# Kernel optimization log

Hardware: AMD Instinct MI355X
Metric: run time of the kernel (lower is better)

Reference implementation:

```python
import jax, jax.numpy as jnp
import numpy as np

B, H, C, PX, PY = 2, 16, 4, 16, 16
EXTRA = 64
HD = 64
N = C * PX * PY + EXTRA


def setup_inputs() -> dict:
    key = jax.random.key(0)
    ks = jax.random.split(key, 8)
    q = jax.random.normal(ks[0], (B, H, N, HD), jnp.float32)
    k = jax.random.normal(ks[1], (B, H, N, HD), jnp.float32)
    v = jax.random.normal(ks[2], (B, H, N, HD), jnp.float32)
    # valid SE(3) world-to-camera matrices: rotation via QR (det fixed to +1)
    A = jax.random.normal(ks[3], (B, C, 3, 3), jnp.float32)
    Q, _ = jnp.linalg.qr(A)
    det = jnp.linalg.det(Q)
    Q = Q * det[..., None, None]
    t = 0.5 * jax.random.normal(ks[4], (B, C, 3), jnp.float32)
    top = jnp.concatenate([Q, t[..., None]], -1)
    bot = jnp.broadcast_to(jnp.array([0.0, 0.0, 0.0, 1.0], jnp.float32), (B, C, 1, 4))
    viewmats = jnp.concatenate([top, bot], -2)
    # pinhole intrinsics (no skew)
    fx = 300.0 + 10.0 * jax.random.uniform(ks[5], (B, C))
    fy = 300.0 + 10.0 * jax.random.uniform(ks[6], (B, C))
    z = jnp.zeros((B, C)); o = jnp.ones((B, C))
    cx = 128.0 * o; cy = 128.0 * o
    Ks = jnp.stack([jnp.stack([fx, z, cx], -1), jnp.stack([z, fy, cy], -1), jnp.stack([z, z, o], -1)], -2)
    spatial_mask = jnp.arange(N) >= EXTRA  # first EXTRA tokens are non-spatial
    return {"q": q, "k": k, "v": v, "viewmats": viewmats, "Ks": Ks,
            "spatial_mask": spatial_mask, "patches_x": PX, "patches_y": PY,
            "image_width": 256, "image_height": 256}


def _invert_SE3(T):
    R = T[..., :3, :3]; t = T[..., :3, 3]
    Rinv = jnp.swapaxes(R, -1, -2)
    tinv = -jnp.einsum('...ij,...j->...i', Rinv, t)
    top = jnp.concatenate([Rinv, tinv[..., None]], -1)
    bot = jnp.broadcast_to(jnp.array([0.0, 0.0, 0.0, 1.0], T.dtype), T.shape[:-2] + (1, 4))
    return jnp.concatenate([top, bot], -2)


def _lift(K3):
    out = jnp.zeros(K3.shape[:-2] + (4, 4), K3.dtype)
    return out.at[..., :3, :3].set(K3).at[..., 3, 3].set(1.0)


def _invert_K(K):
    fx = K[..., 0, 0]; fy = K[..., 1, 1]; cx = K[..., 0, 2]; cy = K[..., 1, 2]
    z = jnp.zeros_like(fx); o = jnp.ones_like(fx)
    return jnp.stack([jnp.stack([1.0 / fx, z, -cx / fx], -1),
                      jnp.stack([z, 1.0 / fy, -cy / fy], -1),
                      jnp.stack([z, z, o], -1)], -2)


def _transform(feats, M, cosx, sinx, cosy, siny, inverse):
    # Block-diagonal: [tiled 4x4 projmat on D/2 | RoPE-x on D/4 | RoPE-y on D/4]
    Bq, Hq, Nq, D = feats.shape
    h2 = D // 2; h4 = D // 4
    p = feats[..., :h2].reshape(Bq, Hq, Nq, h2 // 4, 4)
    p = jnp.einsum('bnij,bhnkj->bhnki', M, p).reshape(Bq, Hq, Nq, h2)

    def rope(x, c, s):
        c = c[None, None]; s = s[None, None]  # [1,1,N,nf]
        xa, xb = x[..., : x.shape[-1] // 2], x[..., x.shape[-1] // 2:]
        if inverse:
            return jnp.concatenate([c * xa - s * xb, s * xa + c * xb], -1)
        return jnp.concatenate([c * xa + s * xb, -s * xa + c * xb], -1)

    rx = rope(feats[..., h2:h2 + h4], cosx, sinx)
    ry = rope(feats[..., h2 + h4:], cosy, siny)
    return jnp.concatenate([p, rx, ry], -1)


def reference(q, k, v, viewmats, Ks, spatial_mask, patches_x, patches_y, image_width, image_height):
    D = q.shape[-1]
    Bq, Cq = viewmats.shape[:2]
    # normalized intrinsics
    fx = Ks[..., 0, 0] / image_width; fy = Ks[..., 1, 1] / image_height
    cx = Ks[..., 0, 2] / image_width - 0.5; cy = Ks[..., 1, 2] / image_height - 0.5
    z = jnp.zeros_like(fx); o = jnp.ones_like(fx)
    Kn = jnp.stack([jnp.stack([fx, z, cx], -1), jnp.stack([z, fy, cy], -1), jnp.stack([z, z, o], -1)], -2)
    P = jnp.einsum('...ij,...jk->...ik', _lift(Kn), viewmats)          # [B,C,4,4]
    P_T = jnp.swapaxes(P, -1, -2)
    P_inv = jnp.einsum('...ij,...jk->...ik', _invert_SE3(viewmats), _lift(_invert_K(Kn)))
    # RoPE tables over spatial tokens (split convention, base=100, scale=1)
    nf = D // 8
    freqs = 100.0 ** (-jnp.arange(nf, dtype=jnp.float32) / nf)
    pos_x = jnp.tile(jnp.arange(patches_x, dtype=jnp.float32), patches_y * Cq)
    pos_y = jnp.tile(jnp.repeat(jnp.arange(patches_y, dtype=jnp.float32), patches_x), Cq)
    ang_x = pos_x[:, None] * freqs; ang_y = pos_y[:, None] * freqs  # [S,nf]
    mask = spatial_mask
    S = pos_x.shape[0]
    # index of each token within the spatial-token ordering (masked scatter, vectorized)
    sidx = jnp.clip(jnp.cumsum(mask.astype(jnp.int32)) - 1, 0, S - 1)
    m = mask[:, None]
    cosx = jnp.where(m, jnp.cos(ang_x)[sidx], 1.0); sinx = jnp.where(m, jnp.sin(ang_x)[sidx], 0.0)
    cosy = jnp.where(m, jnp.cos(ang_y)[sidx], 1.0); siny = jnp.where(m, jnp.sin(ang_y)[sidx], 0.0)
    cam = sidx // (patches_x * patches_y)  # camera id per token
    I4 = jnp.eye(4, dtype=q.dtype)
    mm = mask[None, :, None, None]
    Mq = jnp.where(mm, P_T[:, cam], I4)    # [B,N,4,4]
    Mkv = jnp.where(mm, P_inv[:, cam], I4)
    Mo = jnp.where(mm, P[:, cam], I4)
    qt = _transform(q, Mq, cosx, sinx, cosy, siny, False)
    kt = _transform(k, Mkv, cosx, sinx, cosy, siny, False)
    vt = _transform(v, Mkv, cosx, sinx, cosy, siny, False)
    logits = jnp.einsum('bhqd,bhkd->bhqk', qt, kt) / jnp.sqrt(jnp.float32(D))
    attn = jax.nn.softmax(logits, axis=-1)
    out = jnp.einsum('bhqk,bhkd->bhqd', attn, vt)
    return _transform(out, Mo, cosx, sinx, cosy, siny, True)
```

## Files before the change

kernel.cpp:

```cpp
#include <hip/hip_runtime.h>
#include <math.h>

typedef _Float16 f16;
typedef _Float16 f16x8 __attribute__((ext_vector_type(8)));
typedef __fp16 h16x2 __attribute__((ext_vector_type(2)));
typedef float f32x16 __attribute__((ext_vector_type(16)));
typedef unsigned int u32;
typedef u32 u32x4 __attribute__((ext_vector_type(4)));

constexpr int Bc = 2, Hc = 16, Cc = 4, PXc = 16, PYc = 16, EXTRAc = 64, HDc = 64;
constexpr int Nc = Cc * PXc * PYc + EXTRAc;
constexpr int BH = Bc * Hc;
constexpr int KT = 64;
constexpr int NKT = Nc / KT;
constexpr int KS = 4;
constexpr int NQT = Nc / 32;
constexpr int NBLK = NQT * BH * KS;

constexpr size_t TENS_SZ  = (size_t)BH * Nc * HDc * 2;
constexpr size_t PBH      = (size_t)Nc * 128;
constexpr size_t QF_OFF   = 0;
constexpr size_t KF_OFF   = QF_OFF + TENS_SZ;
constexpr size_t VT_OFF   = KF_OFF + TENS_SZ;
constexpr size_t PART_OFF = VT_OFF + TENS_SZ;
constexpr size_t ML_OFF   = PART_OFF + (size_t)KS * TENS_SZ;

__device__ const float FREQS[8] = {1.0f, 0.5623413252f, 0.31622776601f, 0.17782794100f,
                                   0.1f, 0.05623413252f, 0.031622776602f, 0.017782794100f};
constexpr float QSCALE = 0.125f * 1.4426950408889634f;

__device__ __forceinline__ void compute_M(float* M, const float* __restrict__ vm,
                                          const float* __restrict__ Ks3, int b, int cam, int which) {
    const float* V  = vm + (b * Cc + cam) * 16;
    const float* K3 = Ks3 + (b * Cc + cam) * 9;
    float fx = K3[0] * (1.0f / 256.0f);
    float fy = K3[4] * (1.0f / 256.0f);
    float cx = K3[2] * (1.0f / 256.0f) - 0.5f;
    float cy = K3[5] * (1.0f / 256.0f) - 0.5f;
    if (which == 2) {
        float IV[16];
        IV[0] = V[0]; IV[1] = V[4]; IV[2] = V[8];
        IV[4] = V[1]; IV[5] = V[5]; IV[6] = V[9];
        IV[8] = V[2]; IV[9] = V[6]; IV[10] = V[10];
        float tx = V[3], ty = V[7], tz = V[11];
        IV[3]  = -(IV[0] * tx + IV[1] * ty + IV[2] * tz);
        IV[7]  = -(IV[4] * tx + IV[5] * ty + IV[6] * tz);
        IV[11] = -(IV[8] * tx + IV[9] * ty + IV[10] * tz);
        IV[12] = 0.f; IV[13] = 0.f; IV[14] = 0.f; IV[15] = 1.f;
        float ifx = 1.f / fx, ify = 1.f / fy;
        float ncx = -cx * ifx, ncy = -cy * ify;
        #pragma unroll
        for (int i = 0; i < 4; ++i) {
            M[i * 4 + 0] = IV[i * 4 + 0] * ifx;
            M[i * 4 + 1] = IV[i * 4 + 1] * ify;
            M[i * 4 + 2] = IV[i * 4 + 0] * ncx + IV[i * 4 + 1] * ncy + IV[i * 4 + 2];
            M[i * 4 + 3] = IV[i * 4 + 3];
        }
    } else {
        float P[16];
        #pragma unroll
        for (int j = 0; j < 4; ++j) {
            P[0 * 4 + j] = fx * V[0 * 4 + j] + cx * V[2 * 4 + j];
            P[1 * 4 + j] = fy * V[1 * 4 + j] + cy * V[2 * 4 + j];
            P[2 * 4 + j] = V[2 * 4 + j];
            P[3 * 4 + j] = V[3 * 4 + j];
        }
        if (which == 0) {
            #pragma unroll
            for (int i = 0; i < 16; ++i) M[i] = P[i];
        } else {
            #pragma unroll
            for (int i = 0; i < 4; ++i)
                #pragma unroll
                for (int j = 0; j < 4; ++j) M[i * 4 + j] = P[j * 4 + i];
        }
    }
}

template <bool INV>
__device__ __forceinline__ void xf_seg(float* v16, int seg, int n, int b, int which,
                                       const float* __restrict__ vm, const float* __restrict__ Ks3) {
    if (n < EXTRAc) return;
    int sidx = n - EXTRAc;
    int cam = sidx >> 8;
    if (seg < 2) {
        float M[16];
        compute_M(M, vm, Ks3, b, cam, which);
        #pragma unroll
        for (int g = 0; g < 4; ++g) {
            float a0 = v16[4 * g], a1 = v16[4 * g + 1], a2 = v16[4 * g + 2], a3 = v16[4 * g + 3];
            v16[4 * g + 0] = M[0]  * a0 + M[1]  * a1 + M[2]  * a2 + M[3]  * a3;
            v16[4 * g + 1] = M[4]  * a0 + M[5]  * a1 + M[6]  * a2 + M[7]  * a3;
            v16[4 * g + 2] = M[8]  * a0 + M[9]  * a1 + M[10] * a2 + M[11] * a3;
            v16[4 * g + 3] = M[12] * a0 + M[13] * a1 + M[14] * a2 + M[15] * a3;
        }
    } else {
        float pos = (seg == 2) ? (float)(sidx & (PXc - 1)) : (float)((sidx >> 4) & (PYc - 1));
        #pragma unroll
        for (int f = 0; f < 8; ++f) {
            float s, c;
            __sincosf(pos * FREQS[f], &s, &c);
            float xa = v16[f], xb = v16[8 + f];
            if (INV) {
                v16[f]     = c * xa - s * xb;
                v16[8 + f] = s * xa + c * xb;
            } else {
                v16[f]     = c * xa + s * xb;
                v16[8 + f] = -s * xa + c * xb;
            }
        }
    }
}

__device__ __forceinline__ u32 pkh(float a, float b) {
    h16x2 r = __builtin_amdgcn_cvt_pkrtz(a, b);
    return __builtin_bit_cast(u32, r);
}

__device__ __forceinline__ f32x16 zero16() {
    f32x16 z = {0.f,0.f,0.f,0.f,0.f,0.f,0.f,0.f,0.f,0.f,0.f,0.f,0.f,0.f,0.f,0.f};
    return z;
}

__global__ void prope_xform_kernel(const float* __restrict__ q, const float* __restrict__ k,
                                   const float* __restrict__ v,
                                   const float* __restrict__ viewmats, const float* __restrict__ Ks,
                                   char* __restrict__ wsb) {
    __shared__ f16 tile[64][72];
    if (blockIdx.x < 1088) {
        int id = blockIdx.x * 256 + threadIdx.x;
        int seg = id & 3;
        int rid = id >> 2;
        int tensor = rid / (BH * Nc);
        int row = rid - tensor * (BH * Nc);
        int n = row % Nc;
        int bhq = row / Nc;
        int b = bhq >> 4;
        const float* src = (tensor ? k : q) + (size_t)row * 64 + seg * 16;
        float vals[16];
        #pragma unroll
        for (int i = 0; i < 4; ++i) ((float4*)vals)[i] = ((const float4*)src)[i];
        xf_seg<false>(vals, seg, n, b, tensor ? 2 : 1, viewmats, Ks);
        float scale = tensor ? 1.0f : QSCALE;
        f16 o[16];
        #pragma unroll
        for (int i = 0; i < 16; ++i) o[i] = (f16)(vals[i] * scale);
        if (tensor == 0) {
            char* base = wsb + QF_OFF + (size_t)bhq * PBH + (size_t)(n >> 5) * 4096;
            int qq = n & 31;
            *(float4*)(base + (seg * 2 + 0) * 512 + qq * 16) = ((float4*)o)[0];
            *(float4*)(base + (seg * 2 + 1) * 512 + qq * 16) = ((float4*)o)[1];
        } else {
            char* base = wsb + KF_OFF + (size_t)bhq * PBH + (size_t)(n >> 6) * 8192;
            int kk = n & 63, rh = kk >> 5, qq = kk & 31;
            *(float4*)(base + (((seg * 2 + rh) * 2 + 0) * 32 + qq) * 16) = ((float4*)o)[0];
            *(float4*)(base + (((seg * 2 + rh) * 2 + 1) * 32 + qq) * 16) = ((float4*)o)[1];
        }
    } else {
        int vb = blockIdx.x - 1088;
        int kt = vb >> 5, bh = vb & 31;
        int b = bh >> 4;
        int t = threadIdx.x;
        {
            int r = t >> 2, seg = t & 3;
            int n = kt * 64 + r;
            const float* src = v + ((size_t)bh * Nc + n) * 64 + seg * 16;
            float vals[16];
            #pragma unroll
            for (int i = 0; i < 4; ++i) ((float4*)vals)[i] = ((const float4*)src)[i];
            xf_seg<false>(vals, seg, n, b, 2, viewmats, Ks);
            #pragma unroll
            for (int i = 0; i < 16; ++i) tile[r][seg * 16 + i] = (f16)vals[i];
        }
        __syncthreads();
        {
            int d = t >> 2, ks = t & 3;
            f16 o[16];
            #pragma unroll
            for (int j = 0; j < 16; ++j) o[j] = tile[ks * 16 + j][d];
            int dh = d >> 5, dq = d & 31;
            char* base = wsb + VT_OFF + (size_t)bh * PBH + (size_t)kt * 8192;
            *(float4*)(base + (((ks * 2 + dh) * 2 + 0) * 32 + dq) * 16) = ((float4*)o)[0];
            *(float4*)(base + (((ks * 2 + dh) * 2 + 1) * 32 + dq) * 16) = ((float4*)o)[1];
        }
    }
}

struct KF { f16x8 a0[4]; f16x8 a1[4]; };

__device__ __forceinline__ void load_kf(KF& kf, const char* kb, int lane) {
    #pragma unroll
    for (int c = 0; c < 4; ++c) {
        kf.a0[c] = *(const f16x8*)(kb + (c * 2 + 0) * 1024 + lane * 16);
        kf.a1[c] = *(const f16x8*)(kb + (c * 2 + 1) * 1024 + lane * 16);
    }
}

__device__ __forceinline__ void tile_step(
    const KF& kc, KF& kn, bool pre, const char* vb, const char* kbn,
    const f16x8 (&qb)[4], int lane, int h,
    f32x16& o0, f32x16& o1, float& mrun, float& lrun)
{
    f32x16 s0 = zero16(), s1 = zero16();
    __builtin_amdgcn_s_setprio(1);
    #pragma unroll
    for (int c = 0; c < 4; ++c) {
        s0 = __builtin_amdgcn_mfma_f32_32x32x16_f16(kc.a0[c], qb[c], s0, 0, 0, 0);
        s1 = __builtin_amdgcn_mfma_f32_32x32x16_f16(kc.a1[c], qb[c], s1, 0, 0, 0);
    }
    __builtin_amdgcn_s_setprio(0);
    if (pre) load_kf(kn, kbn, lane);
    f16x8 va0[4], va1[4];
    #pragma unroll
    for (int c = 0; c < 4; ++c) {
        va0[c] = *(const f16x8*)(vb + (c * 2 + 0) * 1024 + lane * 16);
        va1[c] = *(const f16x8*)(vb + (c * 2 + 1) * 1024 + lane * 16);
    }

    float q8[8];
    #pragma unroll
    for (int i = 0; i < 4; ++i) {
        q8[i]     = fmaxf(fmaxf(s0[4*i], s0[4*i+1]), fmaxf(s0[4*i+2], s0[4*i+3]));
        q8[4 + i] = fmaxf(fmaxf(s1[4*i], s1[4*i+1]), fmaxf(s1[4*i+2], s1[4*i+3]));
    }
    float tm = fmaxf(fmaxf(fmaxf(q8[0], q8[1]), fmaxf(q8[2], q8[3])),
                     fmaxf(fmaxf(q8[4], q8[5]), fmaxf(q8[6], q8[7])));
    tm = fmaxf(tm, __shfl_xor(tm, 32, 64));
    if (!__all(tm <= mrun + 8.0f)) {
        float nm = fmaxf(mrun, tm);
        float corr = exp2f(mrun - nm);
        mrun = nm;
        lrun *= corr;
        #pragma unroll
        for (int i = 0; i < 16; ++i) { o0[i] *= corr; o1[i] *= corr; }
    }
    #pragma unroll
    for (int i = 0; i < 16; ++i) s0[i] = exp2f(s0[i] - mrun);
    #pragma unroll
    for (int i = 0; i < 16; ++i) s1[i] = exp2f(s1[i] - mrun);
    float a8[8];
    #pragma unroll
    for (int i = 0; i < 4; ++i) {
        a8[i]     = (s0[4*i] + s0[4*i+1]) + (s0[4*i+2] + s0[4*i+3]);
        a8[4 + i] = (s1[4*i] + s1[4*i+1]) + (s1[4*i+2] + s1[4*i+3]);
    }
    float ps = ((a8[0] + a8[1]) + (a8[2] + a8[3])) + ((a8[4] + a8[5]) + (a8[6] + a8[7]));
    ps += __shfl_xor(ps, 32, 64);
    lrun += ps;

    u32 U0[8], U1[8];
    #pragma unroll
    for (int g = 0; g < 4; ++g) {
        U0[g * 2 + 0] = pkh(s0[4 * g + 0], s0[4 * g + 1]);
        U0[g * 2 + 1] = pkh(s0[4 * g + 2], s0[4 * g + 3]);
        U1[g * 2 + 0] = pkh(s1[4 * g + 0], s1[4 * g + 1]);
        U1[g * 2 + 1] = pkh(s1[4 * g + 2], s1[4 * g + 3]);
    }

    #pragma unroll
    for (int c = 0; c < 4; ++c) {
        const u32* Us = (c < 2) ? U0 : U1;
        int gl = 2 * (c & 1);
        u32 x0 = Us[(gl + 1) * 2 + 0], x1 = Us[(gl + 1) * 2 + 1];
        u32 y0 = Us[gl * 2 + 0],       y1 = Us[gl * 2 + 1];
        u32 s0w = h ? y0 : x0;
        u32 s1w = h ? y1 : x1;
        u32 r0 = (u32)__shfl_xor((int)s0w, 32, 64);
        u32 r1 = (u32)__shfl_xor((int)s1w, 32, 64);
        u32 own0 = h ? x0 : y0, own1 = h ? x1 : y1;
        u32 w0 = h ? r0 : own0;
        u32 w1 = h ? r1 : own1;
        u32 w2 = h ? own0 : r0;
        u32 w3 = h ? own1 : r1;
        u32x4 fw = {w0, w1, w2, w3};
        f16x8 pb = __builtin_bit_cast(f16x8, fw);
        __builtin_amdgcn_s_setprio(1);
        o0 = __builtin_amdgcn_mfma_f32_32x32x16_f16(va0[c], pb, o0, 0, 0, 0);
        o1 = __builtin_amdgcn_mfma_f32_32x32x16_f16(va1[c], pb, o1, 0, 0, 0);
        __builtin_amdgcn_s_setprio(0);
    }
}

__global__ __launch_bounds__(64, 2) void prope_attn_mfma_kernel(
    const char* __restrict__ wsb, char* __restrict__ partO, float* __restrict__ partML) {
    __shared__ char ob[4096];

    const int lane = threadIdx.x;
    const int q = lane & 31, h = lane >> 5;
    const int bid = blockIdx.x;
    const int l = (bid & 7) * (NBLK / 8) + (bid >> 3);
    const int qt = l % NQT;
    const int r  = l / NQT;
    const int bh = r & 31, z = r >> 5;
    const int ts = (NKT * z) / KS, te = (NKT * (z + 1)) / KS;

    const char* kfb = wsb + KF_OFF + (size_t)bh * PBH;
    const char* vfb = wsb + VT_OFF + (size_t)bh * PBH;
    const char* qfb = wsb + QF_OFF + (size_t)bh * PBH + (size_t)qt * 4096;

    f16x8 qb[4];
    #pragma unroll
    for (int c = 0; c < 4; ++c) qb[c] = *(const f16x8*)(qfb + c * 1024 + lane * 16);

    f32x16 o0 = zero16(), o1 = zero16();
    float mrun = -1e30f, lrun = 0.f;

    KF kA, kB;
    load_kf(kA, kfb + (size_t)ts * 8192, lane);
    int it = ts;
    for (;;) {
        tile_step(kA, kB, it + 1 < te, vfb + (size_t)it * 8192,
                  kfb + (size_t)(it + 1) * 8192, qb, lane, h, o0, o1, mrun, lrun);
        if (++it >= te) break;
        tile_step(kB, kA, it + 1 < te, vfb + (size_t)it * 8192,
                  kfb + (size_t)(it + 1) * 8192, qb, lane, h, o0, o1, mrun, lrun);
        if (++it >= te) break;
    }

    float invl = 1.f / lrun;
    #pragma unroll
    for (int g = 0; g < 4; ++g) {
        #pragma unroll
        for (int w = 0; w < 2; ++w) {
            u32 u0 = pkh(o0[4 * g + 2 * w] * invl, o0[4 * g + 2 * w + 1] * invl);
            u32 u1 = pkh(o1[4 * g + 2 * w] * invl, o1[4 * g + 2 * w + 1] * invl);
            int col0 = 16 * g + 8 * h + 4 * w;
            *(u32*)(ob + ((q * 128 + col0) ^ ((q & 7) << 4))) = u0;
            *(u32*)(ob + ((q * 128 + col0 + 64) ^ ((q & 7) << 4))) = u1;
        }
    }
    if (h == 0) {
        float2 mlv = {mrun, lrun};
        ((float2*)partML)[((size_t)z * BH + bh) * Nc + qt * 32 + q] = mlv;
    }
    __syncthreads();
    {
        int rr = lane >> 1, half = lane & 1;
        char* dst = partO + (((size_t)z * BH + bh) * Nc + qt * 32 + rr) * 128 + half * 64;
        #pragma unroll
        for (int j = 0; j < 4; ++j) {
            float4 val = *(float4*)(ob + ((rr * 128 + half * 64 + j * 16) ^ ((rr & 7) << 4)));
            ((float4*)dst)[j] = val;
        }
    }
}

__global__ void prope_combine_kernel(const char* __restrict__ wsb,
                                     const float* __restrict__ viewmats, const float* __restrict__ Ks,
                                     float* __restrict__ out) {
    int id = blockIdx.x * 256 + threadIdx.x;
    int seg = id & 3, rid = id >> 2;
    int n = rid % Nc, bh = rid / Nc, b = bh >> 4;
    const float2* ml = (const float2*)(wsb + ML_OFF);
    float m[KS], l[KS];
    float mstar = -1e30f;
    #pragma unroll
    for (int s = 0; s < KS; ++s) {
        float2 v = ml[((size_t)s * BH + bh) * Nc + n];
        m[s] = v.x; l[s] = v.y;
        mstar = fmaxf(mstar, m[s]);
    }
    float wsum = 0.f, wgt[KS];
    #pragma unroll
    for (int s = 0; s < KS; ++s) { wgt[s] = exp2f(m[s] - mstar) * l[s]; wsum += wgt[s]; }
    float inv = 1.f / wsum;
    float acc[16];
    #pragma unroll
    for (int i = 0; i < 16; ++i) acc[i] = 0.f;
    #pragma unroll
    for (int s = 0; s < KS; ++s) {
        const char* op = wsb + PART_OFF + (((size_t)s * BH + bh) * Nc + n) * 128 + seg * 32;
        f16x8 a0 = *(const f16x8*)op;
        f16x8 a1 = *(const f16x8*)(op + 16);
        #pragma unroll
        for (int i = 0; i < 8; ++i) acc[i] += wgt[s] * (float)a0[i];
        #pragma unroll
        for (int i = 0; i < 8; ++i) acc[8 + i] += wgt[s] * (float)a1[i];
    }
    #pragma unroll
    for (int i = 0; i < 16; ++i) acc[i] *= inv;
    xf_seg<true>(acc, seg, n, b, 0, viewmats, Ks);
    float* go = out + ((size_t)bh * Nc + n) * 64 + seg * 16;
    #pragma unroll
    for (int i = 0; i < 4; ++i) ((float4*)go)[i] = ((const float4*)acc)[i];
}

extern "C" void kernel_launch(void* const* d_in, const int* in_sizes, int n_in,
                              void* d_out, int out_size, void* d_ws, size_t ws_size,
                              hipStream_t stream) {
    const float* q        = (const float*)d_in[0];
    const float* k        = (const float*)d_in[1];
    const float* v        = (const float*)d_in[2];
    const float* viewmats = (const float*)d_in[3];
    const float* Ks       = (const float*)d_in[4];
    char* wsb  = (char*)d_ws;
    float* out = (float*)d_out;

    prope_xform_kernel<<<1088 + 544, 256, 0, stream>>>(q, k, v, viewmats, Ks, wsb);
    prope_attn_mfma_kernel<<<NBLK, 64, 0, stream>>>(wsb, wsb + PART_OFF,
                                                    (float*)(wsb + ML_OFF));
    prope_combine_kernel<<<(BH * Nc * 4) / 256, 256, 0, stream>>>(wsb, viewmats, Ks, out);
}
```

Measured before the change: 50.64 us.

## Split each block's KV range across four waves with in-block LDS merge

Each attention block now runs four waves instead of one. Each wave processes about one quarter of the block's KV tiles (16 splits in total), and the partial outputs are merged through shared memory with a log-sum-exp rescale before the normalized partial is written out. The explicit K-tile double-buffer prefetch is dropped, and the K and V loads are issued together at the start of each tile step. The intent is to hide memory latency through more concurrent waves rather than software pipelining, at the cost of extra LDS traffic, a block-wide barrier, and a serial merge done by wave 0.

```diff
diff --git a/kernel.cpp b/kernel.cpp
--- a/kernel.cpp
+++ b/kernel.cpp
@@ -14,6 +14,7 @@
 constexpr int KT = 64;
 constexpr int NKT = Nc / KT;
 constexpr int KS = 4;
+constexpr int NSPLIT = 16;
 constexpr int NQT = Nc / 32;
 constexpr int NBLK = NQT * BH * KS;
 
@@ -186,36 +187,27 @@
     }
 }
 
-struct KF { f16x8 a0[4]; f16x8 a1[4]; };
-
-__device__ __forceinline__ void load_kf(KF& kf, const char* kb, int lane) {
-    #pragma unroll
-    for (int c = 0; c < 4; ++c) {
-        kf.a0[c] = *(const f16x8*)(kb + (c * 2 + 0) * 1024 + lane * 16);
-        kf.a1[c] = *(const f16x8*)(kb + (c * 2 + 1) * 1024 + lane * 16);
-    }
-}
-
 __device__ __forceinline__ void tile_step(
-    const KF& kc, KF& kn, bool pre, const char* vb, const char* kbn,
-    const f16x8 (&qb)[4], int lane, int h,
+    const char* kb, const char* vb, const f16x8 (&qb)[4], int lane, int h,
     f32x16& o0, f32x16& o1, float& mrun, float& lrun)
 {
+    f16x8 ka0[4], ka1[4], va0[4], va1[4];
+    #pragma unroll
+    for (int c = 0; c < 4; ++c) {
+        ka0[c] = *(const f16x8*)(kb + (c * 2 + 0) * 1024 + lane * 16);
+        ka1[c] = *(const f16x8*)(kb + (c * 2 + 1) * 1024 + lane * 16);
+        va0[c] = *(const f16x8*)(vb + (c * 2 + 0) * 1024 + lane * 16);
+        va1[c] = *(const f16x8*)(vb + (c * 2 + 1) * 1024 + lane * 16);
+    }
+
     f32x16 s0 = zero16(), s1 = zero16();
     __builtin_amdgcn_s_setprio(1);
     #pragma unroll
     for (int c = 0; c < 4; ++c) {
-        s0 = __builtin_amdgcn_mfma_f32_32x32x16_f16(kc.a0[c], qb[c], s0, 0, 0, 0);
-        s1 = __builtin_amdgcn_mfma_f32_32x32x16_f16(kc.a1[c], qb[c], s1, 0, 0, 0);
+        s0 = __builtin_amdgcn_mfma_f32_32x32x16_f16(ka0[c], qb[c], s0, 0, 0, 0);
+        s1 = __builtin_amdgcn_mfma_f32_32x32x16_f16(ka1[c], qb[c], s1, 0, 0, 0);
     }
     __builtin_amdgcn_s_setprio(0);
-    if (pre) load_kf(kn, kbn, lane);
-    f16x8 va0[4], va1[4];
-    #pragma unroll
-    for (int c = 0; c < 4; ++c) {
-        va0[c] = *(const f16x8*)(vb + (c * 2 + 0) * 1024 + lane * 16);
-        va1[c] = *(const f16x8*)(vb + (c * 2 + 1) * 1024 + lane * 16);
-    }
 
     float q8[8];
     #pragma unroll
@@ -257,6 +249,7 @@
         U1[g * 2 + 1] = pkh(s1[4 * g + 2], s1[4 * g + 3]);
     }
 
+    u32 pw[4][4];
     #pragma unroll
     for (int c = 0; c < 4; ++c) {
         const u32* Us = (c < 2) ? U0 : U1;
@@ -268,31 +261,38 @@
         u32 r0 = (u32)__shfl_xor((int)s0w, 32, 64);
         u32 r1 = (u32)__shfl_xor((int)s1w, 32, 64);
         u32 own0 = h ? x0 : y0, own1 = h ? x1 : y1;
-        u32 w0 = h ? r0 : own0;
-        u32 w1 = h ? r1 : own1;
-        u32 w2 = h ? own0 : r0;
-        u32 w3 = h ? own1 : r1;
-        u32x4 fw = {w0, w1, w2, w3};
+        pw[c][0] = h ? r0 : own0;
+        pw[c][1] = h ? r1 : own1;
+        pw[c][2] = h ? own0 : r0;
+        pw[c][3] = h ? own1 : r1;
+    }
+
+    __builtin_amdgcn_s_setprio(1);
+    #pragma unroll
+    for (int c = 0; c < 4; ++c) {
+        u32x4 fw = {pw[c][0], pw[c][1], pw[c][2], pw[c][3]};
         f16x8 pb = __builtin_bit_cast(f16x8, fw);
-        __builtin_amdgcn_s_setprio(1);
         o0 = __builtin_amdgcn_mfma_f32_32x32x16_f16(va0[c], pb, o0, 0, 0, 0);
         o1 = __builtin_amdgcn_mfma_f32_32x32x16_f16(va1[c], pb, o1, 0, 0, 0);
-        __builtin_amdgcn_s_setprio(0);
-    }
-}
-
-__global__ __launch_bounds__(64, 2) void prope_attn_mfma_kernel(
+    }
+    __builtin_amdgcn_s_setprio(0);
+}
+
+__global__ __launch_bounds__(256, 2) void prope_attn_mfma_kernel(
     const char* __restrict__ wsb, char* __restrict__ partO, float* __restrict__ partML) {
-    __shared__ char ob[4096];
-
-    const int lane = threadIdx.x;
+    __shared__ float os[4][32][64];
+    __shared__ float mls[4][2][32];
+
+    const int tid = threadIdx.x;
+    const int wv = tid >> 6, lane = tid & 63;
     const int q = lane & 31, h = lane >> 5;
     const int bid = blockIdx.x;
-    const int l = (bid & 7) * (NBLK / 8) + (bid >> 3);
-    const int qt = l % NQT;
-    const int r  = l / NQT;
-    const int bh = r & 31, z = r >> 5;
-    const int ts = (NKT * z) / KS, te = (NKT * (z + 1)) / KS;
+    const int ll = (bid & 7) * (NBLK / 8) + (bid >> 3);
+    const int qt = ll % NQT;
+    const int rest = ll / NQT;
+    const int bh = rest & 31, z = rest >> 5;
+    const int g = z * 4 + wv;
+    const int ts = (NKT * g) / NSPLIT, te = (NKT * (g + 1)) / NSPLIT;
 
     const char* kfb = wsb + KF_OFF + (size_t)bh * PBH;
     const char* vfb = wsb + VT_OFF + (size_t)bh * PBH;
@@ -305,42 +305,60 @@
     f32x16 o0 = zero16(), o1 = zero16();
     float mrun = -1e30f, lrun = 0.f;
 
-    KF kA, kB;
-    load_kf(kA, kfb + (size_t)ts * 8192, lane);
-    int it = ts;
-    for (;;) {
-        tile_step(kA, kB, it + 1 < te, vfb + (size_t)it * 8192,
-                  kfb + (size_t)(it + 1) * 8192, qb, lane, h, o0, o1, mrun, lrun);
-        if (++it >= te) break;
-        tile_step(kB, kA, it + 1 < te, vfb + (size_t)it * 8192,
-                  kfb + (size_t)(it + 1) * 8192, qb, lane, h, o0, o1, mrun, lrun);
-        if (++it >= te) break;
-    }
-
-    float invl = 1.f / lrun;
-    #pragma unroll
-    for (int g = 0; g < 4; ++g) {
-        #pragma unroll
-        for (int w = 0; w < 2; ++w) {
-            u32 u0 = pkh(o0[4 * g + 2 * w] * invl, o0[4 * g + 2 * w + 1] * invl);
-            u32 u1 = pkh(o1[4 * g + 2 * w] * invl, o1[4 * g + 2 * w + 1] * invl);
-            int col0 = 16 * g + 8 * h + 4 * w;
-            *(u32*)(ob + ((q * 128 + col0) ^ ((q & 7) << 4))) = u0;
-            *(u32*)(ob + ((q * 128 + col0 + 64) ^ ((q & 7) << 4))) = u1;
-        }
-    }
-    if (h == 0) {
-        float2 mlv = {mrun, lrun};
-        ((float2*)partML)[((size_t)z * BH + bh) * Nc + qt * 32 + q] = mlv;
-    }
+    for (int it = ts; it < te; ++it)
+        tile_step(kfb + (size_t)it * 8192, vfb + (size_t)it * 8192,
+                  qb, lane, h, o0, o1, mrun, lrun);
+
+    #pragma unroll
+    for (int i = 0; i < 16; ++i) {
+        os[wv][i][lane]      = o0[i];
+        os[wv][16 + i][lane] = o1[i];
+    }
+    if (h == 0) { mls[wv][0][q] = mrun; mls[wv][1][q] = lrun; }
     __syncthreads();
-    {
-        int rr = lane >> 1, half = lane & 1;
-        char* dst = partO + (((size_t)z * BH + bh) * Nc + qt * 32 + rr) * 128 + half * 64;
-        #pragma unroll
-        for (int j = 0; j < 4; ++j) {
-            float4 val = *(float4*)(ob + ((rr * 128 + half * 64 + j * 16) ^ ((rr & 7) << 4)));
-            ((float4*)dst)[j] = val;
+
+    if (wv == 0) {
+        float m4[4], l4[4];
+        #pragma unroll
+        for (int w = 0; w < 4; ++w) { m4[w] = mls[w][0][q]; l4[w] = mls[w][1][q]; }
+        float mB = fmaxf(fmaxf(m4[0], m4[1]), fmaxf(m4[2], m4[3]));
+        float u4[4], lB = 0.f;
+        #pragma unroll
+        for (int w = 0; w < 4; ++w) { u4[w] = exp2f(m4[w] - mB); lB += u4[w] * l4[w]; }
+        float inv = 1.f / lB;
+        f32x16 a0 = zero16(), a1 = zero16();
+        #pragma unroll
+        for (int w = 0; w < 4; ++w) {
+            #pragma unroll
+            for (int i = 0; i < 16; ++i) {
+                a0[i] += u4[w] * os[w][i][lane];
+                a1[i] += u4[w] * os[w][16 + i][lane];
+            }
+        }
+        char* ob = (char*)os;
+        #pragma unroll
+        for (int gg = 0; gg < 4; ++gg) {
+            #pragma unroll
+            for (int w = 0; w < 2; ++w) {
+                u32 u0 = pkh(a0[4 * gg + 2 * w] * inv, a0[4 * gg + 2 * w + 1] * inv);
+                u32 u1 = pkh(a1[4 * gg + 2 * w] * inv, a1[4 * gg + 2 * w + 1] * inv);
+                int col0 = 16 * gg + 8 * h + 4 * w;
+                *(u32*)(ob + ((q * 128 + col0) ^ ((q & 7) << 4))) = u0;
+                *(u32*)(ob + ((q * 128 + col0 + 64) ^ ((q & 7) << 4))) = u1;
+            }
+        }
+        if (h == 0) {
+            float2 mlv = {mB, lB};
+            ((float2*)partML)[((size_t)z * BH + bh) * Nc + qt * 32 + q] = mlv;
+        }
+        {
+            int rr = lane >> 1, half = lane & 1;
+            char* dst = partO + (((size_t)z * BH + bh) * Nc + qt * 32 + rr) * 128 + half * 64;
+            #pragma unroll
+            for (int j = 0; j < 4; ++j) {
+                float4 val = *(float4*)(ob + ((rr * 128 + half * 64 + j * 16) ^ ((rr & 7) << 4)));
+                ((float4*)dst)[j] = val;
+            }
         }
     }
 }
@@ -397,7 +415,7 @@
     float* out = (float*)d_out;
 
     prope_xform_kernel<<<1088 + 544, 256, 0, stream>>>(q, k, v, viewmats, Ks, wsb);
-    prope_attn_mfma_kernel<<<NBLK, 64, 0, stream>>>(wsb, wsb + PART_OFF,
-                                                    (float*)(wsb + ML_OFF));
+    prope_attn_mfma_kernel<<<NBLK, 256, 0, stream>>>(wsb, wsb + PART_OFF,
+                                                     (float*)(wsb + ML_OFF));
     prope_combine_kernel<<<(BH * Nc * 4) / 256, 256, 0, stream>>>(wsb, viewmats, Ks, out);
 }
```

After: 56.68 us. +11.9%, slower.
